# Performance work log

Hardware: AMD Instinct MI355X
Metric: run time of the kernel (lower is better)

## Reference

```python
import jax, jax.numpy as jnp
import numpy as np

N, IN_F, HID, HEADS, OUT_F, E, G = 20000, 256, 128, 4, 10, 400000, 64
HC = HID * HEADS  # 512


def gatv2_layer(x, src, dst, Wl, bl, Wr, br, att, bias, num_nodes):
    # PyG GATv2Conv (concat=True): lin_l for source msgs, lin_r for targets
    H, C = att.shape
    xl = (x @ Wl + bl).reshape(-1, H, C)
    xr = (x @ Wr + br).reshape(-1, H, C)
    # edge-wise GATv2 score: a^T LeakyReLU(xl_j + xr_i)
    e = jax.nn.leaky_relu(xl[src] + xr[dst], 0.2)          # [E,H,C]
    logits = jnp.einsum('ehc,hc->eh', e, att)              # [E,H]
    # segment softmax over incoming edges of each destination node
    m = jax.ops.segment_max(logits, dst, num_segments=num_nodes)
    p = jnp.exp(logits - m[dst])
    denom = jax.ops.segment_sum(p, dst, num_segments=num_nodes)
    alpha = p / denom[dst]                                 # [E,H]
    out = jax.ops.segment_sum(alpha[:, :, None] * xl[src], dst,
                              num_segments=num_nodes)      # [N,H,C]
    return out.reshape(num_nodes, H * C) + bias


def setup_inputs() -> dict:
    key = jax.random.key(0)
    ks = jax.random.split(key, 32)
    s = 0.05
    inp = {
        'x': jax.random.normal(ks[0], (N, IN_F), jnp.float32),
        'edge_index': jax.random.randint(ks[1], (2, E), 0, N, jnp.int64),
        'batch': jnp.sort(jax.random.randint(ks[2], (N,), 0, G, jnp.int64)),
        'pre_W': jax.random.normal(ks[3], (IN_F, HID), jnp.float32) * s,
        'pre_b': jnp.zeros((HID,), jnp.float32),
        'cls_W': jax.random.normal(ks[4], (HC, OUT_F), jnp.float32) * s,
        'cls_b': jnp.zeros((OUT_F,), jnp.float32),
    }
    in_dims = [HID, HC, HC]
    for i in range(3):
        kk = jax.random.split(ks[5 + i], 6)
        d = in_dims[i]
        inp[f'Wl{i+1}'] = jax.random.normal(kk[0], (d, HC), jnp.float32) * s
        inp[f'bl{i+1}'] = jnp.zeros((HC,), jnp.float32)
        inp[f'Wr{i+1}'] = jax.random.normal(kk[1], (d, HC), jnp.float32) * s
        inp[f'br{i+1}'] = jnp.zeros((HC,), jnp.float32)
        inp[f'att{i+1}'] = jax.random.normal(kk[2], (HEADS, HID), jnp.float32) * s
        inp[f'bias{i+1}'] = jnp.zeros((HC,), jnp.float32)
    return inp


def reference(x, edge_index, batch, pre_W, pre_b, cls_W, cls_b,
              Wl1, bl1, Wr1, br1, att1, bias1,
              Wl2, bl2, Wr2, br2, att2, bias2,
              Wl3, bl3, Wr3, br3, att3, bias3):
    num_nodes = x.shape[0]
    # add self loops (PyG GATv2Conv default)
    loop = jnp.arange(num_nodes, dtype=edge_index.dtype)
    src = jnp.concatenate([edge_index[0], loop])
    dst = jnp.concatenate([edge_index[1], loop])

    h = jax.nn.elu(x @ pre_W + pre_b)  # dropout is identity in eval
    h = jax.nn.elu(gatv2_layer(h, src, dst, Wl1, bl1, Wr1, br1, att1, bias1, num_nodes))
    h = jax.nn.elu(gatv2_layer(h, src, dst, Wl2, bl2, Wr2, br2, att2, bias2, num_nodes))
    h = jax.nn.elu(gatv2_layer(h, src, dst, Wl3, bl3, Wr3, br3, att3, bias3, num_nodes))
    # global mean pool over graphs
    sums = jax.ops.segment_sum(h, batch, num_segments=G)
    cnts = jax.ops.segment_sum(jnp.ones((num_nodes,), h.dtype), batch, num_segments=G)
    pooled = sums / jnp.maximum(cnts, 1.0)[:, None]
    return pooled @ cls_W + cls_b
```

## Files before the change

kernel.cpp:

```cpp
#include <hip/hip_runtime.h>
#include <hip/hip_bf16.h>
#include <math.h>

#define NODES   20000
#define MPAD    20096
#define IN_F    256
#define HID     128
#define HEADS   4
#define OUT_F   10
#define NEDGE   400000
#define NGRAPH  64
#define HC      512
#define EPRIME  (NEDGE + NODES)

typedef __attribute__((ext_vector_type(8))) short bf16x8_t;
typedef __attribute__((ext_vector_type(4))) float f32x4_t;

__device__ __forceinline__ unsigned short bf16_rne(float f) {
    unsigned int u = __float_as_uint(f);
    u += 0x7FFFu + ((u >> 16) & 1u);
    return (unsigned short)(u >> 16);
}
__device__ __forceinline__ float bf16f(unsigned short h) {
    return __uint_as_float(((unsigned int)h) << 16);
}
__device__ __forceinline__ void split2(float f, unsigned short& hi, unsigned short& lo) {
    hi = bf16_rne(f);
    lo = bf16_rne(f - bf16f(hi));
}

#define GLOAD_LDS16(gp, lp) \
    __builtin_amdgcn_global_load_lds((const __attribute__((address_space(1))) unsigned int*)(gp), \
                                     (__attribute__((address_space(3))) unsigned int*)(lp), 16, 0, 0)

__global__ __launch_bounds__(256) void hist_kernel(const int* __restrict__ ei,
                                                   int* __restrict__ counts) {
    int e = blockIdx.x * blockDim.x + threadIdx.x;
    if (e >= EPRIME) return;
    int dst = (e < NEDGE) ? ei[NEDGE + e] : (e - NEDGE);
    atomicAdd(&counts[dst], 1);
}

__global__ __launch_bounds__(1024) void scan_kernel(const int* __restrict__ counts,
                                                    int* __restrict__ offsets,
                                                    int* __restrict__ cursor) {
    __shared__ int wsum[16];
    __shared__ int s_carry;
    const int tid = threadIdx.x;
    const int lane = tid & 63, wid = tid >> 6;
    if (tid == 0) s_carry = 0;
    __syncthreads();
    for (int base = 0; base < NODES; base += 1024) {
        int idx = base + tid;
        int v = (idx < NODES) ? counts[idx] : 0;
        int x = v;
        #pragma unroll
        for (int d = 1; d < 64; d <<= 1) {
            int n = __shfl_up(x, d);
            if (lane >= d) x += n;
        }
        if (lane == 63) wsum[wid] = x;
        __syncthreads();
        if (wid == 0) {
            int w = (lane < 16) ? wsum[lane] : 0;
            #pragma unroll
            for (int d = 1; d < 16; d <<= 1) {
                int n = __shfl_up(w, d);
                if (lane >= d) w += n;
            }
            if (lane < 16) wsum[lane] = w;
        }
        __syncthreads();
        int carry = s_carry;
        int wpre = (wid == 0) ? 0 : wsum[wid - 1];
        int excl = carry + wpre + x - v;
        if (idx < NODES) { offsets[idx] = excl; cursor[idx] = excl; }
        __syncthreads();
        if (tid == 1023) s_carry = carry + wsum[15];
        __syncthreads();
    }
    if (tid == 0) offsets[NODES] = s_carry;
}

__global__ __launch_bounds__(256) void scatter_kernel(const int* __restrict__ ei,
                                                      int* __restrict__ cursor,
                                                      int* __restrict__ srcs) {
    int e = blockIdx.x * blockDim.x + threadIdx.x;
    if (e >= EPRIME) return;
    int src, dst;
    if (e < NEDGE) { src = ei[e]; dst = ei[NEDGE + e]; }
    else           { src = dst = e - NEDGE; }
    int pos = atomicAdd(&cursor[dst], 1);
    srcs[pos] = src;
}

__global__ __launch_bounds__(256) void convert_x_kernel(const float* __restrict__ x,
                                                        unsigned short* __restrict__ x2) {
    int idx = blockIdx.x * 256 + threadIdx.x;
    int r = idx >> 5, g = idx & 31;
    if (r >= MPAD) return;
    __align__(16) unsigned short hv[8], lv[8];
    if (r < NODES) {
        const float* p = &x[(size_t)r * IN_F + g * 8];
        #pragma unroll
        for (int j = 0; j < 8; ++j) split2(p[j], hv[j], lv[j]);
    } else {
        #pragma unroll
        for (int j = 0; j < 8; ++j) { hv[j] = 0; lv[j] = 0; }
    }
    unsigned short* o = x2 + (size_t)r * (2 * IN_F) + g * 16;
    *reinterpret_cast<uint4*>(o)     = *reinterpret_cast<uint4*>(hv);
    *reinterpret_cast<uint4*>(o + 8) = *reinterpret_cast<uint4*>(lv);
}

__global__ __launch_bounds__(256) void convert_w_kernel(const float* __restrict__ W,
                                                        unsigned short* __restrict__ WT2,
                                                        int K, int N, int gshift) {
    int idx = blockIdx.x * 256 + threadIdx.x;
    int n = idx >> gshift, g = idx & ((1 << gshift) - 1);
    if (n >= N) return;
    __align__(16) unsigned short hv[8], lv[8];
    #pragma unroll
    for (int j = 0; j < 8; ++j) split2(W[(size_t)(8 * g + j) * N + n], hv[j], lv[j]);
    unsigned short* o = WT2 + (size_t)n * (2 * K) + g * 16;
    *reinterpret_cast<uint4*>(o)     = *reinterpret_cast<uint4*>(hv);
    *reinterpret_cast<uint4*>(o + 8) = *reinterpret_cast<uint4*>(lv);
}

template <int WRITE_SPLIT, int ACT>
__global__ __launch_bounds__(256) void mfma_gemm_kernel(const unsigned short* __restrict__ A2,
                                                        const unsigned short* __restrict__ B2,
                                                        const float* __restrict__ bias,
                                                        float* __restrict__ Cf,
                                                        unsigned short* __restrict__ C2,
                                                        int M, int N, int K) {
    __shared__ char lds[32768];
    const int tid = threadIdx.x;
    const int w = tid >> 6, l = tid & 63;
    const int wr = w >> 1, wc = w & 1;
    const int row0 = blockIdx.x * 128, col0 = blockIdx.y * 128;
    const size_t rowB = (size_t)K * 4;

    f32x4_t acc[4][4];
    #pragma unroll
    for (int i = 0; i < 4; ++i)
        #pragma unroll
        for (int j = 0; j < 4; ++j)
            #pragma unroll
            for (int q = 0; q < 4; ++q) acc[i][j][q] = 0.f;

    const int ssub = l >> 3;
    const int scol = (l & 7) * 16;
    const int g16  = l >> 4;
    const int fr   = l & 15;

    const char* Ab = (const char*)A2;
    const char* Bb = (const char*)B2;

    const int nsteps = K >> 5;
    for (int t = 0; t < nsteps; ++t) {
        #pragma unroll
        for (int i = 0; i < 4; ++i) {
            int r = w * 32 + i * 8 + ssub;
            size_t gb = (size_t)(row0 + r) * rowB + (size_t)t * 128 + (size_t)(scol ^ ((r & 7) << 4));
            GLOAD_LDS16(Ab + gb, &lds[(w * 32 + i * 8) * 128]);
        }
        #pragma unroll
        for (int i = 0; i < 4; ++i) {
            int r = w * 32 + i * 8 + ssub;
            size_t gb = (size_t)(col0 + r) * rowB + (size_t)t * 128 + (size_t)(scol ^ ((r & 7) << 4));
            GLOAD_LDS16(Bb + gb, &lds[16384 + (w * 32 + i * 8) * 128]);
        }
        asm volatile("s_waitcnt vmcnt(0)" ::: "memory");
        __syncthreads();

        bf16x8_t ah[4], al[4];
        #pragma unroll
        for (int i = 0; i < 4; ++i) {
            int r = wr * 64 + i * 16 + fr;
            int sw = (r & 7) << 4;
            ah[i] = *reinterpret_cast<const bf16x8_t*>(&lds[r * 128 + ((g16 * 32) ^ sw)]);
            al[i] = *reinterpret_cast<const bf16x8_t*>(&lds[r * 128 + ((g16 * 32 + 16) ^ sw)]);
        }
        #pragma unroll
        for (int j = 0; j < 4; ++j) {
            int r = wc * 64 + j * 16 + fr;
            int sw = (r & 7) << 4;
            bf16x8_t bh = *reinterpret_cast<const bf16x8_t*>(&lds[16384 + r * 128 + ((g16 * 32) ^ sw)]);
            bf16x8_t bl = *reinterpret_cast<const bf16x8_t*>(&lds[16384 + r * 128 + ((g16 * 32 + 16) ^ sw)]);
            #pragma unroll
            for (int i = 0; i < 4; ++i) {
                acc[i][j] = __builtin_amdgcn_mfma_f32_16x16x32_bf16(ah[i], bh, acc[i][j], 0, 0, 0);
                acc[i][j] = __builtin_amdgcn_mfma_f32_16x16x32_bf16(ah[i], bl, acc[i][j], 0, 0, 0);
                acc[i][j] = __builtin_amdgcn_mfma_f32_16x16x32_bf16(al[i], bh, acc[i][j], 0, 0, 0);
            }
        }
        __syncthreads();
    }

    const int crb  = (l >> 4) * 4;
    const int ccol = l & 15;
    #pragma unroll
    for (int i = 0; i < 4; ++i) {
        #pragma unroll
        for (int jj = 0; jj < 4; ++jj) {
            int rg = row0 + wr * 64 + i * 16 + crb + jj;
            #pragma unroll
            for (int j = 0; j < 4; ++j) {
                int cg = col0 + wc * 64 + j * 16 + ccol;
                float v = acc[i][j][jj] + bias[cg];
                if (ACT) v = v > 0.f ? v : expm1f(v);
                if (WRITE_SPLIT) {
                    unsigned short hi, lo;
                    split2(v, hi, lo);
                    unsigned short* o = C2 + (size_t)rg * (2 * N) + (cg >> 3) * 16 + (cg & 7);
                    o[0] = hi; o[8] = lo;
                } else {
                    if (rg < M) Cf[(size_t)rg * N + cg] = v;
                }
            }
        }
    }
}

__global__ __launch_bounds__(256) void gat_edge_kernel(const float* __restrict__ xl,
                                                       const float* __restrict__ xr,
                                                       const float* __restrict__ att,
                                                       const float* __restrict__ bias,
                                                       const int* __restrict__ offsets,
                                                       const int* __restrict__ srcs,
                                                       unsigned short* __restrict__ h2) {
    const int node = blockIdx.x;
    if (node >= NODES) {
        uint2* o = (uint2*)(h2 + (size_t)node * (2 * HC));
        o[threadIdx.x] = make_uint2(0u, 0u);
        return;
    }
    const int h = threadIdx.x >> 6, lane = threadIdx.x & 63;
    const int c0 = lane * 2;
    const size_t xoff = (size_t)node * HC + h * HID + c0;
    const float2 xrv = *reinterpret_cast<const float2*>(&xr[xoff]);
    const float2 atv = *reinterpret_cast<const float2*>(&att[h * HID + c0]);
    const int beg = offsets[node], end = offsets[node + 1];

    float m = -INFINITY, denom = 0.f, a0 = 0.f, a1 = 0.f;

    for (int e0 = beg; e0 < end; e0 += 4) {
        int nb = end - e0; if (nb > 4) nb = 4;
        int sx[4]; float2 xv[4];
        #pragma unroll
        for (int q = 0; q < 4; ++q) sx[q] = srcs[e0 + ((q < nb) ? q : 0)];
        #pragma unroll
        for (int q = 0; q < 4; ++q)
            xv[q] = *reinterpret_cast<const float2*>(&xl[(size_t)sx[q] * HC + h * HID + c0]);
        #pragma unroll
        for (int q = 0; q < 4; ++q) {
            if (q >= nb) break;
            float v0 = xv[q].x + xrv.x; v0 = fmaxf(v0, 0.2f * v0);
            float v1 = xv[q].y + xrv.y; v1 = fmaxf(v1, 0.2f * v1);
            float p = atv.x * v0 + atv.y * v1;
            #pragma unroll
            for (int off = 32; off; off >>= 1) p += __shfl_xor(p, off);
            if (p > m) {
                float sc = __expf(m - p);
                denom *= sc; a0 *= sc; a1 *= sc; m = p;
            }
            float wgt = __expf(p - m);
            denom += wgt; a0 += wgt * xv[q].x; a1 += wgt * xv[q].y;
        }
    }

    const float inv = 1.f / denom;
    const float2 bv = *reinterpret_cast<const float2*>(&bias[h * HID + c0]);
    float o0 = a0 * inv + bv.x, o1 = a1 * inv + bv.y;
    o0 = o0 > 0.f ? o0 : expm1f(o0);
    o1 = o1 > 0.f ? o1 : expm1f(o1);
    const int c = h * HID + c0;
    unsigned short h0, l0, h1, l1;
    split2(o0, h0, l0); split2(o1, h1, l1);
    unsigned short* o = h2 + (size_t)node * (2 * HC) + (c >> 3) * 16 + (c & 7);
    o[0] = h0; o[1] = h1; o[8] = l0; o[9] = l1;
}

__global__ __launch_bounds__(256) void pool_cls_kernel(const unsigned short* __restrict__ h2,
                                                       const int* __restrict__ batch,
                                                       const float* __restrict__ W,
                                                       const float* __restrict__ cb,
                                                       float* __restrict__ outp) {
    const int g = blockIdx.x;
    __shared__ float pooled[HC];
    int lo = 0, hi = NODES;
    while (lo < hi) { int mid = (lo + hi) >> 1; if (batch[mid] < g) lo = mid + 1; else hi = mid; }
    const int s = lo;
    lo = s; hi = NODES;
    while (lo < hi) { int mid = (lo + hi) >> 1; if (batch[mid] < g + 1) lo = mid + 1; else hi = mid; }
    const int e = lo;

    const int tid = threadIdx.x;
    const int c0 = tid * 2;
    const int boff = ((c0 >> 3) * 16) + (c0 & 7);
    float s0 = 0.f, s1 = 0.f;
    for (int r = s; r < e; ++r) {
        const unsigned short* p = h2 + (size_t)r * (2 * HC) + boff;
        s0 += bf16f(p[0]) + bf16f(p[8]);
        s1 += bf16f(p[1]) + bf16f(p[9]);
    }
    const float invc = (e > s) ? 1.f / (float)(e - s) : 0.f;
    pooled[c0] = s0 * invc; pooled[c0 + 1] = s1 * invc;
    __syncthreads();

    const int lane = tid & 63, wid = tid >> 6;
    for (int o = wid; o < OUT_F; o += 4) {
        float p = 0.f;
        for (int c = lane; c < HC; c += 64) p += pooled[c] * W[c * OUT_F + o];
        #pragma unroll
        for (int off2 = 32; off2; off2 >>= 1) p += __shfl_xor(p, off2);
        if (lane == 0) outp[g * OUT_F + o] = p + cb[o];
    }
}

extern "C" void kernel_launch(void* const* d_in, const int* in_sizes, int n_in,
                              void* d_out, int out_size, void* d_ws, size_t ws_size,
                              hipStream_t stream) {
    const float* x      = (const float*)d_in[0];
    const int*   ei     = (const int*)d_in[1];
    const int*   batch  = (const int*)d_in[2];
    const float* pre_W  = (const float*)d_in[3];
    const float* pre_b  = (const float*)d_in[4];
    const float* cls_W  = (const float*)d_in[5];
    const float* cls_b  = (const float*)d_in[6];
    const float* Wl[3]; const float* bl[3]; const float* Wr[3];
    const float* br[3]; const float* attw[3]; const float* bw[3];
    for (int l = 0; l < 3; ++l) {
        Wl[l]   = (const float*)d_in[7 + 6 * l + 0];
        bl[l]   = (const float*)d_in[7 + 6 * l + 1];
        Wr[l]   = (const float*)d_in[7 + 6 * l + 2];
        br[l]   = (const float*)d_in[7 + 6 * l + 3];
        attw[l] = (const float*)d_in[7 + 6 * l + 4];
        bw[l]   = (const float*)d_in[7 + 6 * l + 5];
    }
    float* outp = (float*)d_out;

    char* ws = (char*)d_ws;
    size_t off = 0;
    auto alloc = [&](size_t b) { char* p = ws + off; off += (b + 255) & ~(size_t)255; return p; };
    float* xlb = (float*)alloc((size_t)NODES * HC * 4);
    float* xrb = (float*)alloc((size_t)NODES * HC * 4);
    unsigned short* h2 = (unsigned short*)alloc((size_t)MPAD * 2 * HC * 2);
    unsigned short* WlT2 = (unsigned short*)alloc((size_t)HC * 2 * HC * 2);
    unsigned short* WrT2 = (unsigned short*)alloc((size_t)HC * 2 * HC * 2);
    unsigned short* preWT2 = (unsigned short*)alloc((size_t)HID * 2 * IN_F * 2);
    int* counts  = (int*)alloc(NODES * 4);
    int* offsets = (int*)alloc((NODES + 1) * 4);
    int* cursor  = (int*)alloc(NODES * 4);
    int* srcs    = (int*)alloc((size_t)EPRIME * 4);
    unsigned short* x2  = (unsigned short*)xlb;
    unsigned short* h2a = h2;

    hipMemsetAsync(counts, 0, NODES * 4, stream);
    hist_kernel<<<(EPRIME + 255) / 256, 256, 0, stream>>>(ei, counts);
    scan_kernel<<<1, 1024, 0, stream>>>(counts, offsets, cursor);
    scatter_kernel<<<(EPRIME + 255) / 256, 256, 0, stream>>>(ei, cursor, srcs);

    convert_x_kernel<<<(MPAD * (IN_F / 8) + 255) / 256, 256, 0, stream>>>(x, x2);
    convert_w_kernel<<<(HID * (IN_F / 8) + 255) / 256, 256, 0, stream>>>(pre_W, preWT2, IN_F, HID, 5);
    convert_w_kernel<<<(HC * (HID / 8) + 255) / 256, 256, 0, stream>>>(Wl[0], WlT2, HID, HC, 4);
    convert_w_kernel<<<(HC * (HID / 8) + 255) / 256, 256, 0, stream>>>(Wr[0], WrT2, HID, HC, 4);

    mfma_gemm_kernel<1, 1><<<dim3(157, 1), 256, 0, stream>>>(x2, preWT2, pre_b,
                                                             nullptr, h2a, NODES, HID, IN_F);

    mfma_gemm_kernel<0, 0><<<dim3(157, 4), 256, 0, stream>>>(h2a, WlT2, bl[0], xlb, nullptr, NODES, HC, HID);
    mfma_gemm_kernel<0, 0><<<dim3(157, 4), 256, 0, stream>>>(h2a, WrT2, br[0], xrb, nullptr, NODES, HC, HID);
    convert_w_kernel<<<(HC * (HC / 8) + 255) / 256, 256, 0, stream>>>(Wl[1], WlT2, HC, HC, 6);
    convert_w_kernel<<<(HC * (HC / 8) + 255) / 256, 256, 0, stream>>>(Wr[1], WrT2, HC, HC, 6);
    gat_edge_kernel<<<MPAD, 256, 0, stream>>>(xlb, xrb, attw[0], bw[0], offsets, srcs, h2);

    mfma_gemm_kernel<0, 0><<<dim3(157, 4), 256, 0, stream>>>(h2, WlT2, bl[1], xlb, nullptr, NODES, HC, HC);
    mfma_gemm_kernel<0, 0><<<dim3(157, 4), 256, 0, stream>>>(h2, WrT2, br[1], xrb, nullptr, NODES, HC, HC);
    convert_w_kernel<<<(HC * (HC / 8) + 255) / 256, 256, 0, stream>>>(Wl[2], WlT2, HC, HC, 6);
    convert_w_kernel<<<(HC * (HC / 8) + 255) / 256, 256, 0, stream>>>(Wr[2], WrT2, HC, HC, 6);
    gat_edge_kernel<<<MPAD, 256, 0, stream>>>(xlb, xrb, attw[1], bw[1], offsets, srcs, h2);

    mfma_gemm_kernel<0, 0><<<dim3(157, 4), 256, 0, stream>>>(h2, WlT2, bl[2], xlb, nullptr, NODES, HC, HC);
    mfma_gemm_kernel<0, 0><<<dim3(157, 4), 256, 0, stream>>>(h2, WrT2, br[2], xrb, nullptr, NODES, HC, HC);
    gat_edge_kernel<<<MPAD, 256, 0, stream>>>(xlb, xrb, attw[2], bw[2], offsets, srcs, h2);

    pool_cls_kernel<<<NGRAPH, 256, 0, stream>>>(h2, batch, cls_W, cls_b, outp);
}
```

Baseline: 955.0 us.

## Fuse Wl/Wr GEMMs, batch edge score reductions, precompute byte offsets, split pooling

Concatenates the Wl and Wr weights so each layer runs a single GEMM that writes an interleaved [N,1024] xl|xr buffer, halving launches and A-matrix reads. The edge kernel stores source indices pre-shifted to byte offsets and folds log2(e) into att so it can use exp2f. It reduces four edge scores at once with a transposed butterfly shuffle and does one online-softmax max update per group of four edges. Pooling is split into a 4-way partial-sum kernel plus a classifier kernel for more parallelism. The interleaved layout doubles the row stride of the gathered xl reads, which may reduce cache locality.

```diff
diff --git a/kernel.cpp b/kernel.cpp
--- a/kernel.cpp
+++ b/kernel.cpp
@@ -12,6 +12,7 @@
 #define NGRAPH  64
 #define HC      512
 #define EPRIME  (NEDGE + NODES)
+#define XLRW    1024
 
 typedef __attribute__((ext_vector_type(8))) short bf16x8_t;
 typedef __attribute__((ext_vector_type(4))) float f32x4_t;
@@ -84,14 +85,14 @@
 
 __global__ __launch_bounds__(256) void scatter_kernel(const int* __restrict__ ei,
                                                       int* __restrict__ cursor,
-                                                      int* __restrict__ srcs) {
+                                                      int* __restrict__ srcsb) {
     int e = blockIdx.x * blockDim.x + threadIdx.x;
     if (e >= EPRIME) return;
     int src, dst;
     if (e < NEDGE) { src = ei[e]; dst = ei[NEDGE + e]; }
     else           { src = dst = e - NEDGE; }
     int pos = atomicAdd(&cursor[dst], 1);
-    srcs[pos] = src;
+    srcsb[pos] = src << 12;
 }
 
 __global__ __launch_bounds__(256) void convert_x_kernel(const float* __restrict__ x,
@@ -125,6 +126,22 @@
     unsigned short* o = WT2 + (size_t)n * (2 * K) + g * 16;
     *reinterpret_cast<uint4*>(o)     = *reinterpret_cast<uint4*>(hv);
     *reinterpret_cast<uint4*>(o + 8) = *reinterpret_cast<uint4*>(lv);
+}
+
+__global__ __launch_bounds__(256) void build_bias_kernel(const float* __restrict__ bl1,
+                                                         const float* __restrict__ br1,
+                                                         const float* __restrict__ bl2,
+                                                         const float* __restrict__ br2,
+                                                         const float* __restrict__ bl3,
+                                                         const float* __restrict__ br3,
+                                                         float* __restrict__ out) {
+    int idx = blockIdx.x * 256 + threadIdx.x;
+    if (idx >= 3 * 1024) return;
+    int l = idx >> 10, c = idx & 1023;
+    const float* p = (l == 0) ? (c < 512 ? bl1 : br1)
+                   : (l == 1) ? (c < 512 ? bl2 : br2)
+                              : (c < 512 ? bl3 : br3);
+    out[idx] = p[c & 511];
 }
 
 template <int WRITE_SPLIT, int ACT>
@@ -223,12 +240,11 @@
     }
 }
 
-__global__ __launch_bounds__(256) void gat_edge_kernel(const float* __restrict__ xl,
-                                                       const float* __restrict__ xr,
+__global__ __launch_bounds__(256) void gat_edge_kernel(const float* __restrict__ xlr,
                                                        const float* __restrict__ att,
                                                        const float* __restrict__ bias,
                                                        const int* __restrict__ offsets,
-                                                       const int* __restrict__ srcs,
+                                                       const int* __restrict__ srcsb,
                                                        unsigned short* __restrict__ h2) {
     const int node = blockIdx.x;
     if (node >= NODES) {
@@ -238,55 +254,110 @@
     }
     const int h = threadIdx.x >> 6, lane = threadIdx.x & 63;
     const int c0 = lane * 2;
-    const size_t xoff = (size_t)node * HC + h * HID + c0;
-    const float2 xrv = *reinterpret_cast<const float2*>(&xr[xoff]);
-    const float2 atv = *reinterpret_cast<const float2*>(&att[h * HID + c0]);
+    const int ch = h * HID + c0;
+    const char* xlb = (const char*)xlr;
+    const int laneoff = ch * 4;
+    const float2 xrv = *reinterpret_cast<const float2*>(&xlr[(size_t)node * XLRW + 512 + ch]);
+    float2 atv = *reinterpret_cast<const float2*>(&att[ch]);
+    atv.x *= 1.44269504f; atv.y *= 1.44269504f;
     const int beg = offsets[node], end = offsets[node + 1];
 
     float m = -INFINITY, denom = 0.f, a0 = 0.f, a1 = 0.f;
+    const bool b5 = (lane & 32) != 0, b4 = (lane & 16) != 0;
 
     for (int e0 = beg; e0 < end; e0 += 4) {
-        int nb = end - e0; if (nb > 4) nb = 4;
-        int sx[4]; float2 xv[4];
-        #pragma unroll
-        for (int q = 0; q < 4; ++q) sx[q] = srcs[e0 + ((q < nb) ? q : 0)];
+        const int nb = min(4, end - e0);
+        int sb[4]; float2 xv[4]; float p[4];
+        #pragma unroll
+        for (int q = 0; q < 4; ++q) sb[q] = srcsb[e0 + ((q < nb) ? q : nb - 1)];
         #pragma unroll
         for (int q = 0; q < 4; ++q)
-            xv[q] = *reinterpret_cast<const float2*>(&xl[(size_t)sx[q] * HC + h * HID + c0]);
+            xv[q] = *reinterpret_cast<const float2*>(xlb + (size_t)(unsigned)sb[q] + laneoff);
         #pragma unroll
         for (int q = 0; q < 4; ++q) {
-            if (q >= nb) break;
             float v0 = xv[q].x + xrv.x; v0 = fmaxf(v0, 0.2f * v0);
             float v1 = xv[q].y + xrv.y; v1 = fmaxf(v1, 0.2f * v1);
-            float p = atv.x * v0 + atv.y * v1;
-            #pragma unroll
-            for (int off = 32; off; off >>= 1) p += __shfl_xor(p, off);
-            if (p > m) {
-                float sc = __expf(m - p);
-                denom *= sc; a0 *= sc; a1 *= sc; m = p;
-            }
-            float wgt = __expf(p - m);
-            denom += wgt; a0 += wgt * xv[q].x; a1 += wgt * xv[q].y;
+            p[q] = fmaf(atv.y, v1, atv.x * v0);
+        }
+        float s0 = b5 ? p[0] : p[2];
+        float u0 = (b5 ? p[2] : p[0]) + __shfl_xor(s0, 32);
+        float s1 = b5 ? p[1] : p[3];
+        float u1 = (b5 ? p[3] : p[1]) + __shfl_xor(s1, 32);
+        float s2 = b4 ? u0 : u1;
+        float t  = (b4 ? u1 : u0) + __shfl_xor(s2, 16);
+        t += __shfl_xor(t, 8);
+        t += __shfl_xor(t, 4);
+        t += __shfl_xor(t, 2);
+        t += __shfl_xor(t, 1);
+        const float pe0 = __shfl(t, 0);
+        const float pe1 = __shfl(t, 16);
+        const float pe2 = __shfl(t, 32);
+        const float pe3 = __shfl(t, 48);
+
+        const float m4 = fmaxf(fmaxf(pe0, pe1), fmaxf(pe2, pe3));
+        if (m4 > m) {
+            float sc = exp2f(m - m4);
+            denom *= sc; a0 *= sc; a1 *= sc; m = m4;
+        }
+        {
+            float w0 = exp2f(pe0 - m);
+            denom += w0; a0 = fmaf(w0, xv[0].x, a0); a1 = fmaf(w0, xv[0].y, a1);
+        }
+        if (nb > 1) {
+            float w1 = exp2f(pe1 - m);
+            denom += w1; a0 = fmaf(w1, xv[1].x, a0); a1 = fmaf(w1, xv[1].y, a1);
+        }
+        if (nb > 2) {
+            float w2 = exp2f(pe2 - m);
+            denom += w2; a0 = fmaf(w2, xv[2].x, a0); a1 = fmaf(w2, xv[2].y, a1);
+        }
+        if (nb > 3) {
+            float w3 = exp2f(pe3 - m);
+            denom += w3; a0 = fmaf(w3, xv[3].x, a0); a1 = fmaf(w3, xv[3].y, a1);
         }
     }
 
     const float inv = 1.f / denom;
-    const float2 bv = *reinterpret_cast<const float2*>(&bias[h * HID + c0]);
+    const float2 bv = *reinterpret_cast<const float2*>(&bias[ch]);
     float o0 = a0 * inv + bv.x, o1 = a1 * inv + bv.y;
     o0 = o0 > 0.f ? o0 : expm1f(o0);
     o1 = o1 > 0.f ? o1 : expm1f(o1);
-    const int c = h * HID + c0;
     unsigned short h0, l0, h1, l1;
     split2(o0, h0, l0); split2(o1, h1, l1);
-    unsigned short* o = h2 + (size_t)node * (2 * HC) + (c >> 3) * 16 + (c & 7);
+    unsigned short* o = h2 + (size_t)node * (2 * HC) + (ch >> 3) * 16 + (ch & 7);
     o[0] = h0; o[1] = h1; o[8] = l0; o[9] = l1;
 }
 
-__global__ __launch_bounds__(256) void pool_cls_kernel(const unsigned short* __restrict__ h2,
-                                                       const int* __restrict__ batch,
-                                                       const float* __restrict__ W,
-                                                       const float* __restrict__ cb,
-                                                       float* __restrict__ outp) {
+__global__ __launch_bounds__(256) void pool_part_kernel(const unsigned short* __restrict__ h2,
+                                                        const int* __restrict__ batch,
+                                                        float* __restrict__ partial) {
+    const int g = blockIdx.x, part = blockIdx.y;
+    int lo = 0, hi = NODES;
+    while (lo < hi) { int mid = (lo + hi) >> 1; if (batch[mid] < g) lo = mid + 1; else hi = mid; }
+    const int s = lo;
+    lo = s; hi = NODES;
+    while (lo < hi) { int mid = (lo + hi) >> 1; if (batch[mid] < g + 1) lo = mid + 1; else hi = mid; }
+    const int e = lo, cnt = e - s;
+    const int ps = s + (cnt * part) / 4;
+    const int pe = s + (cnt * (part + 1)) / 4;
+
+    const int c0 = threadIdx.x * 2;
+    const int boff = ((c0 >> 3) * 16) + (c0 & 7);
+    float s0 = 0.f, s1 = 0.f;
+    for (int r = ps; r < pe; ++r) {
+        const unsigned short* p = h2 + (size_t)r * (2 * HC) + boff;
+        s0 += bf16f(p[0]) + bf16f(p[8]);
+        s1 += bf16f(p[1]) + bf16f(p[9]);
+    }
+    float* o = partial + ((size_t)(g * 4 + part)) * HC;
+    o[c0] = s0; o[c0 + 1] = s1;
+}
+
+__global__ __launch_bounds__(256) void cls_kernel(const float* __restrict__ partial,
+                                                  const int* __restrict__ batch,
+                                                  const float* __restrict__ W,
+                                                  const float* __restrict__ cb,
+                                                  float* __restrict__ outp) {
     const int g = blockIdx.x;
     __shared__ float pooled[HC];
     int lo = 0, hi = NODES;
@@ -294,22 +365,20 @@
     const int s = lo;
     lo = s; hi = NODES;
     while (lo < hi) { int mid = (lo + hi) >> 1; if (batch[mid] < g + 1) lo = mid + 1; else hi = mid; }
-    const int e = lo;
-
-    const int tid = threadIdx.x;
-    const int c0 = tid * 2;
-    const int boff = ((c0 >> 3) * 16) + (c0 & 7);
+    const int cnt = lo - s;
+
+    const int c0 = threadIdx.x * 2;
     float s0 = 0.f, s1 = 0.f;
-    for (int r = s; r < e; ++r) {
-        const unsigned short* p = h2 + (size_t)r * (2 * HC) + boff;
-        s0 += bf16f(p[0]) + bf16f(p[8]);
-        s1 += bf16f(p[1]) + bf16f(p[9]);
-    }
-    const float invc = (e > s) ? 1.f / (float)(e - s) : 0.f;
+    #pragma unroll
+    for (int part = 0; part < 4; ++part) {
+        const float* p = partial + ((size_t)(g * 4 + part)) * HC;
+        s0 += p[c0]; s1 += p[c0 + 1];
+    }
+    const float invc = cnt > 0 ? 1.f / (float)cnt : 0.f;
     pooled[c0] = s0 * invc; pooled[c0 + 1] = s1 * invc;
     __syncthreads();
 
-    const int lane = tid & 63, wid = tid >> 6;
+    const int lane = threadIdx.x & 63, wid = threadIdx.x >> 6;
     for (int o = wid; o < OUT_F; o += 4) {
         float p = 0.f;
         for (int c = lane; c < HC; c += 64) p += pooled[c] * W[c * OUT_F + o];
@@ -344,47 +413,45 @@
     char* ws = (char*)d_ws;
     size_t off = 0;
     auto alloc = [&](size_t b) { char* p = ws + off; off += (b + 255) & ~(size_t)255; return p; };
-    float* xlb = (float*)alloc((size_t)NODES * HC * 4);
-    float* xrb = (float*)alloc((size_t)NODES * HC * 4);
+    float* xlr = (float*)alloc((size_t)MPAD * XLRW * 4);
     unsigned short* h2 = (unsigned short*)alloc((size_t)MPAD * 2 * HC * 2);
-    unsigned short* WlT2 = (unsigned short*)alloc((size_t)HC * 2 * HC * 2);
-    unsigned short* WrT2 = (unsigned short*)alloc((size_t)HC * 2 * HC * 2);
+    unsigned short* WT2f = (unsigned short*)alloc((size_t)1024 * 2 * HC * 2);
     unsigned short* preWT2 = (unsigned short*)alloc((size_t)HID * 2 * IN_F * 2);
+    float* biascat = (float*)alloc(3 * 1024 * 4);
     int* counts  = (int*)alloc(NODES * 4);
     int* offsets = (int*)alloc((NODES + 1) * 4);
     int* cursor  = (int*)alloc(NODES * 4);
-    int* srcs    = (int*)alloc((size_t)EPRIME * 4);
-    unsigned short* x2  = (unsigned short*)xlb;
-    unsigned short* h2a = h2;
+    int* srcsb   = (int*)alloc((size_t)EPRIME * 4);
+    unsigned short* x2 = (unsigned short*)xlr;
+    float* partial = xlr;
 
     hipMemsetAsync(counts, 0, NODES * 4, stream);
     hist_kernel<<<(EPRIME + 255) / 256, 256, 0, stream>>>(ei, counts);
     scan_kernel<<<1, 1024, 0, stream>>>(counts, offsets, cursor);
-    scatter_kernel<<<(EPRIME + 255) / 256, 256, 0, stream>>>(ei, cursor, srcs);
+    scatter_kernel<<<(EPRIME + 255) / 256, 256, 0, stream>>>(ei, cursor, srcsb);
 
     convert_x_kernel<<<(MPAD * (IN_F / 8) + 255) / 256, 256, 0, stream>>>(x, x2);
     convert_w_kernel<<<(HID * (IN_F / 8) + 255) / 256, 256, 0, stream>>>(pre_W, preWT2, IN_F, HID, 5);
-    convert_w_kernel<<<(HC * (HID / 8) + 255) / 256, 256, 0, stream>>>(Wl[0], WlT2, HID, HC, 4);
-    convert_w_kernel<<<(HC * (HID / 8) + 255) / 256, 256, 0, stream>>>(Wr[0], WrT2, HID, HC, 4);
+    build_bias_kernel<<<12, 256, 0, stream>>>(bl[0], br[0], bl[1], br[1], bl[2], br[2], biascat);
+    convert_w_kernel<<<(HC * (HID / 8) + 255) / 256, 256, 0, stream>>>(Wl[0], WT2f, HID, HC, 4);
+    convert_w_kernel<<<(HC * (HID / 8) + 255) / 256, 256, 0, stream>>>(Wr[0], WT2f + (size_t)512 * 2 * HID, HID, HC, 4);
 
     mfma_gemm_kernel<1, 1><<<dim3(157, 1), 256, 0, stream>>>(x2, preWT2, pre_b,
-                                                             nullptr, h2a, NODES, HID, IN_F);
-
-    mfma_gemm_kernel<0, 0><<<dim3(157, 4), 256, 0, stream>>>(h2a, WlT2, bl[0], xlb, nullptr, NODES, HC, HID);
-    mfma_gemm_kernel<0, 0><<<dim3(157, 4), 256, 0, stream>>>(h2a, WrT2, br[0], xrb, nullptr, NODES, HC, HID);
-    convert_w_kernel<<<(HC * (HC / 8) + 255) / 256, 256, 0, stream>>>(Wl[1], WlT2, HC, HC, 6);
-    convert_w_kernel<<<(HC * (HC / 8) + 255) / 256, 256, 0, stream>>>(Wr[1], WrT2, HC, HC, 6);
-    gat_edge_kernel<<<MPAD, 256, 0, stream>>>(xlb, xrb, attw[0], bw[0], offsets, srcs, h2);
-
-    mfma_gemm_kernel<0, 0><<<dim3(157, 4), 256, 0, stream>>>(h2, WlT2, bl[1], xlb, nullptr, NODES, HC, HC);
-    mfma_gemm_kernel<0, 0><<<dim3(157, 4), 256, 0, stream>>>(h2, WrT2, br[1], xrb, nullptr, NODES, HC, HC);
-    convert_w_kernel<<<(HC * (HC / 8) + 255) / 256, 256, 0, stream>>>(Wl[2], WlT2, HC, HC, 6);
-    convert_w_kernel<<<(HC * (HC / 8) + 255) / 256, 256, 0, stream>>>(Wr[2], WrT2, HC, HC, 6);
-    gat_edge_kernel<<<MPAD, 256, 0, stream>>>(xlb, xrb, attw[1], bw[1], offsets, srcs, h2);
-
-    mfma_gemm_kernel<0, 0><<<dim3(157, 4), 256, 0, stream>>>(h2, WlT2, bl[2], xlb, nullptr, NODES, HC, HC);
-    mfma_gemm_kernel<0, 0><<<dim3(157, 4), 256, 0, stream>>>(h2, WrT2, br[2], xrb, nullptr, NODES, HC, HC);
-    gat_edge_kernel<<<MPAD, 256, 0, stream>>>(xlb, xrb, attw[2], bw[2], offsets, srcs, h2);
-
-    pool_cls_kernel<<<NGRAPH, 256, 0, stream>>>(h2, batch, cls_W, cls_b, outp);
-}
+                                                             nullptr, h2, NODES, HID, IN_F);
+
+    mfma_gemm_kernel<0, 0><<<dim3(157, 8), 256, 0, stream>>>(h2, WT2f, biascat, xlr, nullptr, NODES, 1024, HID);
+    convert_w_kernel<<<(HC * (HC / 8) + 255) / 256, 256, 0, stream>>>(Wl[1], WT2f, HC, HC, 6);
+    convert_w_kernel<<<(HC * (HC / 8) + 255) / 256, 256, 0, stream>>>(Wr[1], WT2f + (size_t)512 * 2 * HC, HC, HC, 6);
+    gat_edge_kernel<<<MPAD, 256, 0, stream>>>(xlr, attw[0], bw[0], offsets, srcsb, h2);
+
+    mfma_gemm_kernel<0, 0><<<dim3(157, 8), 256, 0, stream>>>(h2, WT2f, biascat + 1024, xlr, nullptr, NODES, 1024, HC);
+    convert_w_kernel<<<(HC * (HC / 8) + 255) / 256, 256, 0, stream>>>(Wl[2], WT2f, HC, HC, 6);
+    convert_w_kernel<<<(HC * (HC / 8) + 255) / 256, 256, 0, stream>>>(Wr[2], WT2f + (size_t)512 * 2 * HC, HC, HC, 6);
+    gat_edge_kernel<<<MPAD, 256, 0, stream>>>(xlr, attw[1], bw[1], offsets, srcsb, h2);
+
+    mfma_gemm_kernel<0, 0><<<dim3(157, 8), 256, 0, stream>>>(h2, WT2f, biascat + 2048, xlr, nullptr, NODES, 1024, HC);
+    gat_edge_kernel<<<MPAD, 256, 0, stream>>>(xlr, attw[2], bw[2], offsets, srcsb, h2);
+
+    pool_part_kernel<<<dim3(NGRAPH, 4), 256, 0, stream>>>(h2, batch, partial);
+    cls_kernel<<<NGRAPH, 256, 0, stream>>>(partial, batch, cls_W, cls_b, outp);
+}
```

Result: faster. 826.1 us (-13.5%).
